# Optimization experiments

Hardware: AMD Instinct MI355X
Metric: run time of the kernel (lower is better)

The kernel has to match this reference:

```python
import jax, jax.numpy as jnp
import numpy as np

NEG_SLOPE = 0.2
EPS = 1e-16

N_NODES = 32768
N_EDGES = 160000
DIM = 768
HEADS1 = 4
OUT1 = DIM // HEADS1  # 192 per head, concat -> 768
HEADS2 = 1
OUT2 = DIM
N_REL = 3


def setup_inputs() -> dict:
    key = jax.random.key(0)
    ks = jax.random.split(key, 12)
    s = 0.02
    return {
        "x": jax.random.normal(ks[0], (N_NODES, DIM), dtype=jnp.float32),
        "edge_index": jax.random.randint(ks[1], (2, N_EDGES), 0, N_NODES, dtype=jnp.int64),
        "edge_type": jax.random.randint(ks[2], (N_EDGES,), 0, N_REL, dtype=jnp.int64),
        "W1": jax.random.normal(ks[3], (N_REL, DIM, HEADS1 * OUT1), dtype=jnp.float32) * s,
        "q1": jax.random.normal(ks[4], (HEADS1 * OUT1, HEADS1), dtype=jnp.float32) * s,
        "k1": jax.random.normal(ks[5], (HEADS1 * OUT1, HEADS1), dtype=jnp.float32) * s,
        "b1": jnp.zeros((HEADS1 * OUT1,), dtype=jnp.float32),
        "W2": jax.random.normal(ks[6], (N_REL, DIM, HEADS2 * OUT2), dtype=jnp.float32) * s,
        "q2": jax.random.normal(ks[7], (HEADS2 * OUT2, HEADS2), dtype=jnp.float32) * s,
        "k2": jax.random.normal(ks[8], (HEADS2 * OUT2, HEADS2), dtype=jnp.float32) * s,
        "b2": jnp.zeros((HEADS2 * OUT2,), dtype=jnp.float32),
    }


def rgat_conv(x, W, q, k, b, src, dst, etype, heads, out_ch, n_nodes):
    """PyG RGATConv, additive-self-attention, across-relation, concat=True, eval mode."""
    # per-relation transform of all nodes: [R, N, H*O] (avoids [E, in, H*O] weight gather)
    xr = jnp.einsum('nd,rdf->rnf', x, W)
    oi = xr[etype, dst]                      # [E, H*O] transformed target feats
    oj = xr[etype, src]                      # [E, H*O] transformed source feats
    qi = oi @ q                              # [E, H]
    kj = oj @ k                              # [E, H]
    alpha = jax.nn.leaky_relu(qi + kj, NEG_SLOPE)
    # segment softmax over edges sharing the same target node
    m = jax.ops.segment_max(alpha, dst, num_segments=n_nodes)     # [N, H]
    e = jnp.exp(alpha - m[dst])
    z = jax.ops.segment_sum(e, dst, num_segments=n_nodes)         # [N, H]
    a = e / (z[dst] + EPS)                                        # [E, H]
    msg = (a[:, :, None] * oj.reshape(-1, heads, out_ch)).reshape(-1, heads * out_ch)
    out = jax.ops.segment_sum(msg, dst, num_segments=n_nodes)     # [N, H*O]
    return out + b


def reference(x, edge_index, edge_type, W1, q1, k1, b1, W2, q2, k2, b2):
    src, dst = edge_index[0], edge_index[1]
    n = x.shape[0]
    h = rgat_conv(x, W1, q1, k1, b1, src, dst, edge_type, HEADS1, OUT1, n)
    h = jax.nn.elu(h)
    # dropout is identity in eval mode
    out = rgat_conv(h, W2, q2, k2, b2, src, dst, edge_type, HEADS2, OUT2, n)
    return out
```

## Files before the change

### kernel.cpp

```cpp
#include <hip/hip_runtime.h>


#define DIM   768
#define NREL  3

typedef __bf16 bf16x8 __attribute__((ext_vector_type(8)));
typedef float  f32x4  __attribute__((ext_vector_type(4)));
typedef unsigned short us4 __attribute__((ext_vector_type(4)));
typedef unsigned short us8 __attribute__((ext_vector_type(8)));

__device__ __forceinline__ float bfs(unsigned short u){
  union { unsigned u; float f; } v; v.u = ((unsigned)u) << 16; return v.f;
}
__device__ __forceinline__ float bfl(unsigned x){
  union { unsigned u; float f; } v; v.u = x << 16; return v.f;
}
__device__ __forceinline__ float bfh(unsigned x){
  union { unsigned u; float f; } v; v.u = x & 0xffff0000u; return v.f;
}
__device__ __forceinline__ unsigned short f2bf(float f){
  union { float f; unsigned u; } v; v.f = f;
  unsigned r = v.u + 0x7fffu + ((v.u >> 16) & 1u);
  return (unsigned short)(r >> 16);
}
__device__ __forceinline__ unsigned pck(float a, float b){
  return (unsigned)f2bf(a) | ((unsigned)f2bf(b) << 16);
}
__device__ __forceinline__ float ldf(const void* p, size_t i, int is32){
  return is32 ? ((const float*)p)[i] : bfs(((const unsigned short*)p)[i]);
}
__device__ __forceinline__ int ldi(const void* p, size_t i, int is64){
  return is64 ? ((const int*)p)[2 * i] : ((const int*)p)[i];
}

typedef __attribute__((address_space(1))) void gvoid_t;
typedef __attribute__((address_space(3))) void lvoid_t;
__device__ __forceinline__ void gload16(const void* g, void* l){
  __builtin_amdgcn_global_load_lds((gvoid_t*)g, (lvoid_t*)l, 16, 0, 0);
}

template<int H>
__device__ __forceinline__ float sel(const float (&a)[H], int h){
  float v = a[0];
#pragma unroll
  for (int i = 1; i < H; ++i) v = (h == i) ? a[i] : v;
  return v;
}

__global__ void detect_kernel(const unsigned short* __restrict__ xu,
                              const unsigned* __restrict__ eiu,
                              const unsigned* __restrict__ etyu,
                              int* __restrict__ flags){
  __shared__ int s_weird, s_ei, s_ety;
  int t = threadIdx.x;
  if (t == 0){ s_weird = 0; s_ei = 0; s_ety = 0; }
  __syncthreads();
  unsigned short u = xu[2 * t];
  int ex = (u >> 7) & 0xff;
  if (ex >= 0xF0 || ex <= 0x40) atomicAdd(&s_weird, 1);
  if (t < 128){
    if (eiu[2 * t + 1]  != 0) atomicAdd(&s_ei, 1);
    if (etyu[2 * t + 1] != 0) atomicAdd(&s_ety, 1);
  }
  __syncthreads();
  if (t == 0){
    flags[0] = (s_weird > 16) ? 1 : 0;
    flags[1] = (s_ei  == 0) ? 1 : 0;
    flags[2] = (s_ety == 0) ? 1 : 0;
  }
}

__global__ void convert_x(const void* __restrict__ xin, unsigned short* __restrict__ xb,
                          const int* __restrict__ flags, int n4){
  int i = blockIdx.x * blockDim.x + threadIdx.x;
  if (i >= n4) return;
  if (flags[0]){
    float4 v = ((const float4*)xin)[i];
    us4 o; o.x = f2bf(v.x); o.y = f2bf(v.y); o.z = f2bf(v.z); o.w = f2bf(v.w);
    ((us4*)xb)[i] = o;
  } else {
    ((us4*)xb)[i] = ((const us4*)xin)[i];
  }
}

__global__ void hist_kernel(const void* __restrict__ ei, int* __restrict__ counts,
                            const int* __restrict__ flags, int E){
  int e = blockIdx.x * blockDim.x + threadIdx.x;
  if (e < E) atomicAdd(&counts[ldi(ei, (size_t)E + e, flags[1])], 1);
}

__global__ void scan_kernel(const int* __restrict__ counts, int* __restrict__ offs,
                            int* __restrict__ cursor, int n){
  __shared__ int s[1024];
  int tid = threadIdx.x;
  int base = tid * 32;
  int loc[32];
  int run = 0;
#pragma unroll
  for (int i = 0; i < 32; ++i){ loc[i] = run; run += counts[base + i]; }
  s[tid] = run;
  __syncthreads();
  for (int off = 1; off < 1024; off <<= 1){
    int add = (tid >= off) ? s[tid - off] : 0;
    __syncthreads();
    s[tid] += add;
    __syncthreads();
  }
  int ex = (tid == 0) ? 0 : s[tid - 1];
#pragma unroll
  for (int i = 0; i < 32; ++i){
    int o = ex + loc[i];
    offs[base + i]   = o;
    cursor[base + i] = o;
  }
  if (tid == 1023) offs[n] = s[1023];
}

__global__ void scatter_kernel(const void* __restrict__ ei, const void* __restrict__ ety,
                               int* __restrict__ cursor, int* __restrict__ payload,
                               const int* __restrict__ flags, int E){
  int e = blockIdx.x * blockDim.x + threadIdx.x;
  if (e < E){
    int dst = ldi(ei, (size_t)E + e, flags[1]);
    int src = ldi(ei, (size_t)e,     flags[1]);
    int et  = ldi(ety, (size_t)e,    flags[2]);
    int pos = atomicAdd(&cursor[dst], 1);
    payload[pos] = (et << 16) | src;
  }
}

__global__ void transpose_w(const void* __restrict__ W, unsigned short* __restrict__ Wt,
                            const int* __restrict__ flags){
  __shared__ unsigned short t[32][33];
  int is32 = flags[0];
  int r = blockIdx.z;
  size_t Wb = (size_t)r * DIM * DIM;
  unsigned short* Wd = Wt + (size_t)r * DIM * DIM;
  int tx = threadIdx.x, ty = threadIdx.y;
  int x  = blockIdx.x * 32 + tx;
  int y0 = blockIdx.y * 32;
#pragma unroll
  for (int i = 0; i < 32; i += 8)
    t[ty + i][tx] = f2bf(ldf(W, Wb + (size_t)(y0 + ty + i) * DIM + x, is32));
  __syncthreads();
  int x2 = blockIdx.y * 32 + tx;
  int y2 = blockIdx.x * 32;
#pragma unroll
  for (int i = 0; i < 32; i += 8) Wd[(size_t)(y2 + ty + i) * DIM + x2] = t[tx][ty + i];
}

template<int H>
__global__ void wqk_kernel(const void* __restrict__ W,
                           const void* __restrict__ q, const void* __restrict__ k,
                           unsigned short* __restrict__ Wqkb,
                           const int* __restrict__ flags){
  int is32 = flags[0];
  int wid  = (blockIdx.x * blockDim.x + threadIdx.x) >> 6;
  int lane = threadIdx.x & 63;
  int r = wid / DIM, d = wid % DIM;
  size_t Wrow = ((size_t)r * DIM + d) * DIM;
  float aq[H], ak[H];
#pragma unroll
  for (int h = 0; h < H; ++h){ aq[h] = 0.f; ak[h] = 0.f; }
#pragma unroll
  for (int j = 0; j < 12; ++j){
    int f = j * 64 + lane;
    float wv = ldf(W, Wrow + f, is32);
#pragma unroll
    for (int h = 0; h < H; ++h){
      aq[h] += wv * ldf(q, (size_t)f * H + h, is32);
      ak[h] += wv * ldf(k, (size_t)f * H + h, is32);
    }
  }
#pragma unroll
  for (int h = 0; h < H; ++h){
    for (int off = 32; off; off >>= 1){
      aq[h] += __shfl_xor(aq[h], off);
      ak[h] += __shfl_xor(ak[h], off);
    }
  }
  if (lane == 0){
#pragma unroll
    for (int h = 0; h < H; ++h){
      Wqkb[(size_t)d * 32 + r * 8 + h]     = f2bf(aq[h]);
      Wqkb[(size_t)d * 32 + r * 8 + 4 + h] = f2bf(ak[h]);
    }
  }
}

__global__ void pack_b(const unsigned short* __restrict__ Wqkb, unsigned short* __restrict__ Bpk){
  int i = blockIdx.x * 256 + threadIdx.x;
  if (i >= 3072) return;
  int lane = i & 63, nt = (i >> 6) & 1, t = i >> 7;
  int kb = t * 32 + (lane >> 4) * 8;
  int col = nt * 16 + (lane & 15);
  us8 v;
#pragma unroll
  for (int j = 0; j < 8; ++j) v[j] = Wqkb[(size_t)(kb + j) * 32 + col];
  ((us8*)Bpk)[i] = v;
}

__global__ void __launch_bounds__(256)
qnkn_mfma(const unsigned short* __restrict__ X, const unsigned short* __restrict__ Bpk,
          float* __restrict__ qn, float* __restrict__ kn, int nN){
  int wv = threadIdx.x >> 6, lane = threadIdx.x & 63;
  int row0 = (blockIdx.x * 4 + wv) * 16;
  int ar = lane & 15, quad = lane >> 4;
  const unsigned short* Arow = X + (size_t)(row0 + ar) * DIM + quad * 8;
  const bf16x8* Bp = (const bf16x8*)Bpk;
  f32x4 acc0 = {0.f,0.f,0.f,0.f}, acc1 = {0.f,0.f,0.f,0.f};
#pragma unroll
  for (int t = 0; t < 24; ++t){
    bf16x8 a  = *(const bf16x8*)(Arow + t * 32);
    bf16x8 b0 = Bp[(t * 2 + 0) * 64 + lane];
    bf16x8 b1 = Bp[(t * 2 + 1) * 64 + lane];
    acc0 = __builtin_amdgcn_mfma_f32_16x16x32_bf16(a, b0, acc0, 0, 0, 0);
    acc1 = __builtin_amdgcn_mfma_f32_16x16x32_bf16(a, b1, acc1, 0, 0, 0);
  }
#pragma unroll
  for (int nt = 0; nt < 2; ++nt){
    int col = nt * 16 + (lane & 15);
    if (col < 24){
      int r = col >> 3, isK = (col >> 2) & 1, h = col & 3;
      float* bp = isK ? kn : qn;
      f32x4 a = nt ? acc1 : acc0;
#pragma unroll
      for (int j = 0; j < 4; ++j){
        int row = row0 + quad * 4 + j;
        bp[((size_t)r * nN + row) * 4 + h] = a[j];
      }
    }
  }
}

#define MM4(mi, av) \
    acc[mi][0] = __builtin_amdgcn_mfma_f32_16x16x32_bf16(av, b0, acc[mi][0], 0, 0, 0); \
    acc[mi][1] = __builtin_amdgcn_mfma_f32_16x16x32_bf16(av, b1, acc[mi][1], 0, 0, 0); \
    acc[mi][2] = __builtin_amdgcn_mfma_f32_16x16x32_bf16(av, b2, acc[mi][2], 0, 0, 0); \
    acc[mi][3] = __builtin_amdgcn_mfma_f32_16x16x32_bf16(av, b3, acc[mi][3], 0, 0, 0);

__global__ void __launch_bounds__(512, 2)
gemm_bf16(const unsigned short* __restrict__ A,
          const unsigned short* __restrict__ Bt,
          unsigned short* __restrict__ C, int M){
  __shared__ __align__(16) unsigned char lds[131072];
  const int K = DIM;
  int i = blockIdx.x;
  int xcd = i & 7, s = i >> 3;
  int bm  = xcd * 16 + s / 9;
  int bnr = s % 9;
  int rrel = bnr / 3, bn = bnr % 3;
  int tid = threadIdx.x;
  int w = tid >> 6, lane = tid & 63;
  int wr = w >> 2, wc = w & 3;
  int m16 = lane & 15, quad = lane >> 4;

  int jlow = m16 >> 1;
  int p    = (((m16 & 1) << 2) | quad) ^ jlow;
  int aoff = (wr * 64 + jlow) * 128 + p * 16;
  int boff = (wc * 32 + jlow) * 128 + p * 16;

  int sq = (lane & 7) ^ (lane >> 3);
  int rb = 2 * (w * 16 + (lane >> 3)) + (sq >> 2);
  const unsigned short* gA = A  + (size_t)(bm * 256 + rb) * K + (sq & 3) * 8;
  const unsigned short* gB = Bt + ((size_t)(rrel * DIM + bn * 256 + rb)) * K + (sq & 3) * 8;
  int dstbase = w * 2048;

  f32x4 acc[8][4];
#pragma unroll
  for (int a = 0; a < 8; ++a)
#pragma unroll
    for (int b = 0; b < 4; ++b) acc[a][b] = (f32x4){0.f, 0.f, 0.f, 0.f};

  auto STAGE = [&](int op, int kk, int dbuf, int k0){
    const unsigned short* g = op ? gB : gA;
#pragma unroll
    for (int it = 0; it < 2; ++it)
      gload16(g + (size_t)(it * 16) * K + kk * 32 + k0,
              &lds[(((dbuf << 2) | (op << 1) | kk) << 14) + dstbase + it * 1024]);
  };
  auto LDA = [&](int kk, int cb, int mi) -> bf16x8 {
    return *(const bf16x8*)&lds[(((cb << 2) | kk) << 14) + aoff + mi * 1024];
  };
  auto LDB = [&](int kk, int cb, int ni) -> bf16x8 {
    return *(const bf16x8*)&lds[(((cb << 2) | 2 | kk) << 14) + boff + ni * 1024];
  };

  auto KTILE = [&](int cb, int k0, int sN, int s2){
    bf16x8 b0, b1, b2, b3, a0, a1, a2, a3;
    b0 = LDB(0, cb, 0); b1 = LDB(0, cb, 1); b2 = LDB(0, cb, 2); b3 = LDB(0, cb, 3);
    a0 = LDA(0, cb, 0); a1 = LDA(0, cb, 1); a2 = LDA(0, cb, 2); a3 = LDA(0, cb, 3);
    if (sN) STAGE(0, 1, cb ^ 1, k0 + 64);
    __builtin_amdgcn_s_barrier();
    __builtin_amdgcn_s_setprio(1);
    MM4(0, a0) MM4(1, a1) MM4(2, a2) MM4(3, a3)
    __builtin_amdgcn_s_setprio(0);
    __builtin_amdgcn_s_barrier();
    a0 = LDA(0, cb, 4); a1 = LDA(0, cb, 5); a2 = LDA(0, cb, 6); a3 = LDA(0, cb, 7);
    if (s2) STAGE(1, 0, cb, k0 + 128);
    __builtin_amdgcn_s_barrier();
    __builtin_amdgcn_s_setprio(1);
    MM4(4, a0) MM4(5, a1) MM4(6, a2) MM4(7, a3)
    __builtin_amdgcn_s_setprio(0);
    __builtin_amdgcn_s_barrier();
    b0 = LDB(1, cb, 0); b1 = LDB(1, cb, 1); b2 = LDB(1, cb, 2); b3 = LDB(1, cb, 3);
    a0 = LDA(1, cb, 0); a1 = LDA(1, cb, 1); a2 = LDA(1, cb, 2); a3 = LDA(1, cb, 3);
    if (s2) STAGE(0, 0, cb, k0 + 128);
    __builtin_amdgcn_s_barrier();
    __builtin_amdgcn_s_setprio(1);
    MM4(0, a0) MM4(1, a1) MM4(2, a2) MM4(3, a3)
    __builtin_amdgcn_s_setprio(0);
    __builtin_amdgcn_s_barrier();
    a0 = LDA(1, cb, 4); a1 = LDA(1, cb, 5); a2 = LDA(1, cb, 6); a3 = LDA(1, cb, 7);
    if (s2) STAGE(1, 1, cb, k0 + 128);
    __builtin_amdgcn_s_barrier();
    __builtin_amdgcn_s_setprio(1);
    MM4(4, a0) MM4(5, a1) MM4(6, a2) MM4(7, a3)
    __builtin_amdgcn_s_setprio(0);
  };

  STAGE(1, 0, 0, 0);  STAGE(0, 0, 0, 0);  STAGE(1, 1, 0, 0);  STAGE(0, 1, 0, 0);
  STAGE(1, 0, 1, 64); STAGE(0, 0, 1, 64); STAGE(1, 1, 1, 64);
  asm volatile("s_waitcnt vmcnt(6)");
  __builtin_amdgcn_s_barrier();

#pragma unroll 1
  for (int it = 0; it < 5; ++it){
    int k0 = it * 128;
    KTILE(0, k0, 1, 1);
    asm volatile("s_waitcnt vmcnt(6)");
    __builtin_amdgcn_s_barrier();
    KTILE(1, k0 + 64, 1, 1);
    asm volatile("s_waitcnt vmcnt(6)");
    __builtin_amdgcn_s_barrier();
  }
  KTILE(0, 640, 1, 0);
  asm volatile("s_waitcnt vmcnt(0)");
  __builtin_amdgcn_s_barrier();
  KTILE(1, 704, 0, 0);

  unsigned short* Cg = C + ((size_t)rrel * M + (size_t)bm * 256) * DIM + bn * 256;
#pragma unroll
  for (int mi = 0; mi < 8; ++mi)
#pragma unroll
    for (int ni = 0; ni < 4; ++ni){
#pragma unroll
      for (int j = 0; j < 4; ++j){
        int row = wr * 128 + mi * 16 + quad * 4 + j;
        int col = wc * 64 + ni * 16 + m16;
        Cg[(size_t)row * DIM + col] = f2bf(acc[mi][ni][j]);
      }
    }
}

template<int H, bool ELU, bool OUT32>
__global__ void __launch_bounds__(256)
agg_kernel(const unsigned short* __restrict__ xr,
           const float* __restrict__ qn, const float* __restrict__ kn,
           const int* __restrict__ offs, const int* __restrict__ payload,
           const void* __restrict__ bias,
           void* __restrict__ outp,
           const int* __restrict__ flags, int nN, int E){
  const int WH = (H == 4) ? 4 : 1;
  __shared__ int   pay_s[4][64];
  __shared__ float w_s[4][64 * WH];
  int is32 = flags[0];
  int wv   = threadIdx.x >> 6;
  int lane = threadIdx.x & 63;
  int n = blockIdx.x * 4 + wv;
  int rs = offs[n], re = offs[n + 1];
  rs = max(rs, 0); re = min(re, E);
  const int myh = (H == 1) ? 0 : (lane >> 4);

  float m_run[H], z_run[H], acc[12];
#pragma unroll
  for (int h = 0; h < H; ++h){ m_run[h] = -__builtin_inff(); z_run[h] = 0.f; }
#pragma unroll
  for (int i = 0; i < 12; ++i) acc[i] = 0.f;

  for (int base = rs; base < re; base += 64){
    int dc = min(64, re - base);
    int pay = 0;
    float al[H];
#pragma unroll
    for (int h = 0; h < H; ++h) al[h] = -__builtin_inff();
    if (lane < dc){
      pay = payload[base + lane];
      int et = pay >> 16, src = pay & 0xffff;
      if (H == 4){
        f32x4 qv = *(const f32x4*)(qn + ((size_t)et * nN + n)   * 4);
        f32x4 kv = *(const f32x4*)(kn + ((size_t)et * nN + src) * 4);
#pragma unroll
        for (int h = 0; h < H; ++h){
          float a = qv[h & 3] + kv[h & 3];
          al[h] = (a > 0.f) ? a : 0.2f * a;
        }
      } else {
        float a = qn[((size_t)et * nN + n) * 4] + kn[((size_t)et * nN + src) * 4];
        al[0] = (a > 0.f) ? a : 0.2f * a;
      }
    }
    float scs[H], wgt[H];
#pragma unroll
    for (int h = 0; h < H; ++h){
      float v = al[h];
      for (int off = 32; off; off >>= 1) v = fmaxf(v, __shfl_xor(v, off));
      float nm = fmaxf(m_run[h], v);
      scs[h] = (m_run[h] == -__builtin_inff()) ? 0.f : expf(m_run[h] - nm);
      m_run[h] = nm;
      wgt[h] = (lane < dc) ? expf(al[h] - nm) : 0.f;
      float s = wgt[h];
      for (int off = 32; off; off >>= 1) s += __shfl_xor(s, off);
      z_run[h] = z_run[h] * scs[h] + s;
    }
    float msc = sel<H>(scs, myh);
#pragma unroll
    for (int i = 0; i < 12; ++i) acc[i] *= msc;

    if (lane < dc){
      pay_s[wv][lane] = pay;
#pragma unroll
      for (int h = 0; h < WH; ++h) w_s[wv][lane * WH + h] = wgt[h];
    }

    for (int j0 = 0; j0 < dc; j0 += 4){
      uint2 c[4][3];
      float w4[4];
#pragma unroll
      for (int u = 0; u < 4; ++u){
        int jc = j0 + u;
        int ok = jc < dc;
        int jl = ok ? jc : j0;
        int pj = pay_s[wv][jl];
        float ww = w_s[wv][jl * WH + ((H == 1) ? 0 : myh)];
        w4[u] = ok ? ww : 0.f;
        int et = pj >> 16, src = pj & 0xffff;
        const uint2* rp = (const uint2*)(xr + ((size_t)et * nN + src) * DIM + lane * 12);
        c[u][0] = rp[0]; c[u][1] = rp[1]; c[u][2] = rp[2];
      }
#pragma unroll
      for (int u = 0; u < 4; ++u){
        float wj = w4[u];
        acc[0]  += wj * bfl(c[u][0].x); acc[1]  += wj * bfh(c[u][0].x);
        acc[2]  += wj * bfl(c[u][0].y); acc[3]  += wj * bfh(c[u][0].y);
        acc[4]  += wj * bfl(c[u][1].x); acc[5]  += wj * bfh(c[u][1].x);
        acc[6]  += wj * bfl(c[u][1].y); acc[7]  += wj * bfh(c[u][1].y);
        acc[8]  += wj * bfl(c[u][2].x); acc[9]  += wj * bfh(c[u][2].x);
        acc[10] += wj * bfl(c[u][2].y); acc[11] += wj * bfh(c[u][2].y);
      }
    }
  }

  float inv = 1.0f / (sel<H>(z_run, myh) + 1e-16f);
  float o[12];
#pragma unroll
  for (int i = 0; i < 12; ++i){
    float v = acc[i] * inv + ldf(bias, (size_t)lane * 12 + i, is32);
    if (ELU) v = (v > 0.f) ? v : (expf(v) - 1.f);
    o[i] = v;
  }
  if (OUT32 && is32){
    float* op = (float*)outp + (size_t)n * DIM + lane * 12;
    float4 f0 = {o[0], o[1], o[2],  o[3]};
    float4 f1 = {o[4], o[5], o[6],  o[7]};
    float4 f2 = {o[8], o[9], o[10], o[11]};
    ((float4*)op)[0] = f0; ((float4*)op)[1] = f1; ((float4*)op)[2] = f2;
  } else {
    uint2* op = (uint2*)((unsigned short*)outp + (size_t)n * DIM + lane * 12);
    uint2 s0, s1, s2;
    s0.x = pck(o[0], o[1]);  s0.y = pck(o[2], o[3]);
    s1.x = pck(o[4], o[5]);  s1.y = pck(o[6], o[7]);
    s2.x = pck(o[8], o[9]);  s2.y = pck(o[10], o[11]);
    op[0] = s0; op[1] = s1; op[2] = s2;
  }
}

extern "C" void kernel_launch(void* const* d_in, const int* in_sizes, int n_in,
                              void* d_out, int out_size, void* d_ws, size_t ws_size,
                              hipStream_t stream){
  const void* x   = d_in[0];
  const void* ei  = d_in[1];
  const void* ety = d_in[2];
  const void* W1  = d_in[3];
  const void* q1  = d_in[4];
  const void* k1  = d_in[5];
  const void* b1  = d_in[6];
  const void* W2  = d_in[7];
  const void* q2  = d_in[8];
  const void* k2  = d_in[9];
  const void* b2  = d_in[10];

  int nN = in_sizes[0] / DIM;
  int E  = in_sizes[2];

  char* ws = (char*)d_ws;
  size_t off = 0;
  auto alloc = [&](size_t bytes) -> void* {
    void* p = ws + off;
    off += (bytes + 255) & ~(size_t)255;
    return p;
  };
  unsigned short* xr   = (unsigned short*)alloc((size_t)NREL * nN * DIM * 2);
  unsigned short* xb   = (unsigned short*)alloc((size_t)nN * DIM * 2);
  unsigned short* h    = (unsigned short*)alloc((size_t)nN * DIM * 2);
  unsigned short* Wt   = (unsigned short*)alloc((size_t)NREL * DIM * DIM * 2);
  unsigned short* Wqkb = (unsigned short*)alloc((size_t)DIM * 32 * 2);
  unsigned short* Bpk  = (unsigned short*)alloc((size_t)3072 * 16);
  float* qn  = (float*)alloc((size_t)NREL * nN * 4 * 4);
  float* kn  = (float*)alloc((size_t)NREL * nN * 4 * 4);
  int* offs    = (int*)alloc((size_t)(nN + 1) * 4);
  int* cursor  = (int*)alloc((size_t)nN * 4);
  int* counts  = (int*)alloc((size_t)nN * 4);
  int* payload = (int*)alloc((size_t)E * 4);
  int* flags   = (int*)alloc(16);

  detect_kernel<<<1, 256, 0, stream>>>((const unsigned short*)x, (const unsigned*)ei,
                                       (const unsigned*)ety, flags);
  convert_x<<<(nN * DIM / 4 + 255) / 256, 256, 0, stream>>>(x, xb, flags, nN * DIM / 4);

  hipMemsetAsync(counts, 0, (size_t)nN * 4, stream);
  hist_kernel<<<(E + 255) / 256, 256, 0, stream>>>(ei, counts, flags, E);
  scan_kernel<<<1, 1024, 0, stream>>>(counts, offs, cursor, nN);
  scatter_kernel<<<(E + 255) / 256, 256, 0, stream>>>(ei, ety, cursor, payload, flags, E);

  dim3 tg(DIM / 32, DIM / 32, NREL), tb(32, 8);
  int gemm_blocks = 8 * (16 * 9);

  transpose_w<<<tg, tb, 0, stream>>>(W1, Wt, flags);
  hipMemsetAsync(Wqkb, 0, (size_t)DIM * 32 * 2, stream);
  wqk_kernel<4><<<(NREL * DIM) / 4, 256, 0, stream>>>(W1, q1, k1, Wqkb, flags);
  pack_b<<<12, 256, 0, stream>>>(Wqkb, Bpk);
  qnkn_mfma<<<nN / 64, 256, 0, stream>>>(xb, Bpk, qn, kn, nN);
  gemm_bf16<<<gemm_blocks, 512, 0, stream>>>(xb, Wt, xr, nN);
  agg_kernel<4, true, false><<<nN / 4, 256, 0, stream>>>(xr, qn, kn, offs, payload, b1, h,
                                                         flags, nN, E);

  transpose_w<<<tg, tb, 0, stream>>>(W2, Wt, flags);
  hipMemsetAsync(Wqkb, 0, (size_t)DIM * 32 * 2, stream);
  wqk_kernel<1><<<(NREL * DIM) / 4, 256, 0, stream>>>(W2, q2, k2, Wqkb, flags);
  pack_b<<<12, 256, 0, stream>>>(Wqkb, Bpk);
  qnkn_mfma<<<nN / 64, 256, 0, stream>>>(h, Bpk, qn, kn, nN);
  gemm_bf16<<<gemm_blocks, 512, 0, stream>>>(h, Wt, xr, nN);
  agg_kernel<1, false, true><<<nN / 4, 256, 0, stream>>>(xr, qn, kn, offs, payload, b2,
                                                         d_out, flags, nN, E);
}
```

Measured before the change: 677.9 us.

## Shrink GEMM tile to 128x256 with triple-buffered 32-wide K pipeline

Halves the GEMM M-tile from 256 to 128 rows, so each of the 8 waves holds a 4x4 accumulator array instead of 8x4. The K-loop now steps by 32 through a three-slot LDS ring, with one stage in flight while another is computed. LDS use drops from 128 KB to 72 KB and launch bounds request 4 blocks per CU, aiming at higher occupancy and better latency hiding. In exchange, each tile reuses its B data over fewer rows, it needs more barriers per unit of K, and twice as many blocks are launched.

```diff
diff --git a/kernel.cpp b/kernel.cpp
--- a/kernel.cpp
+++ b/kernel.cpp
@@ -239,15 +239,15 @@
     acc[mi][2] = __builtin_amdgcn_mfma_f32_16x16x32_bf16(av, b2, acc[mi][2], 0, 0, 0); \
     acc[mi][3] = __builtin_amdgcn_mfma_f32_16x16x32_bf16(av, b3, acc[mi][3], 0, 0, 0);
 
-__global__ void __launch_bounds__(512, 2)
+__global__ void __launch_bounds__(512, 4)
 gemm_bf16(const unsigned short* __restrict__ A,
           const unsigned short* __restrict__ Bt,
           unsigned short* __restrict__ C, int M){
-  __shared__ __align__(16) unsigned char lds[131072];
+  __shared__ __align__(16) unsigned char lds[73728];
   const int K = DIM;
   int i = blockIdx.x;
   int xcd = i & 7, s = i >> 3;
-  int bm  = xcd * 16 + s / 9;
+  int bm  = xcd * 32 + s / 9;
   int bnr = s % 9;
   int rrel = bnr / 3, bn = bnr % 3;
   int tid = threadIdx.x;
@@ -257,96 +257,76 @@
 
   int jlow = m16 >> 1;
   int p    = (((m16 & 1) << 2) | quad) ^ jlow;
-  int aoff = (wr * 64 + jlow) * 128 + p * 16;
+  int aoff = (wr * 32 + jlow) * 128 + p * 16;
   int boff = (wc * 32 + jlow) * 128 + p * 16;
 
-  int sq = (lane & 7) ^ (lane >> 3);
-  int rb = 2 * (w * 16 + (lane >> 3)) + (sq >> 2);
-  const unsigned short* gA = A  + (size_t)(bm * 256 + rb) * K + (sq & 3) * 8;
-  const unsigned short* gB = Bt + ((size_t)(rrel * DIM + bn * 256 + rb)) * K + (sq & 3) * 8;
-  int dstbase = w * 2048;
-
-  f32x4 acc[8][4];
-#pragma unroll
-  for (int a = 0; a < 8; ++a)
+  int sq  = (tid & 7) ^ ((tid >> 3) & 7);
+  int rb  = 2 * (tid >> 3) + (sq >> 2);
+  const unsigned short* gA  = A  + (size_t)(bm * 128 + rb) * K + (sq & 3) * 8;
+  const unsigned short* gB0 = Bt + ((size_t)(rrel * DIM + bn * 256 + rb)) * K + (sq & 3) * 8;
+  const unsigned short* gB1 = gB0 + (size_t)128 * K;
+  unsigned char* dst = &lds[w * 1024];
+
+  f32x4 acc[4][4];
+#pragma unroll
+  for (int a = 0; a < 4; ++a)
 #pragma unroll
     for (int b = 0; b < 4; ++b) acc[a][b] = (f32x4){0.f, 0.f, 0.f, 0.f};
 
-  auto STAGE = [&](int op, int kk, int dbuf, int k0){
-    const unsigned short* g = op ? gB : gA;
-#pragma unroll
-    for (int it = 0; it < 2; ++it)
-      gload16(g + (size_t)(it * 16) * K + kk * 32 + k0,
-              &lds[(((dbuf << 2) | (op << 1) | kk) << 14) + dstbase + it * 1024]);
+  auto STAGE = [&](int slot, int k0){
+    unsigned char* base = dst + slot * 24576;
+    gload16(gA  + k0, base);
+    gload16(gB0 + k0, base + 8192);
+    gload16(gB1 + k0, base + 16384);
   };
-  auto LDA = [&](int kk, int cb, int mi) -> bf16x8 {
-    return *(const bf16x8*)&lds[(((cb << 2) | kk) << 14) + aoff + mi * 1024];
+  auto LDA = [&](int slot, int mi) -> bf16x8 {
+    return *(const bf16x8*)&lds[slot * 24576 + aoff + mi * 1024];
   };
-  auto LDB = [&](int kk, int cb, int ni) -> bf16x8 {
-    return *(const bf16x8*)&lds[(((cb << 2) | 2 | kk) << 14) + boff + ni * 1024];
+  auto LDB = [&](int slot, int ni) -> bf16x8 {
+    return *(const bf16x8*)&lds[slot * 24576 + 8192 + boff + ni * 1024];
   };
-
-  auto KTILE = [&](int cb, int k0, int sN, int s2){
-    bf16x8 b0, b1, b2, b3, a0, a1, a2, a3;
-    b0 = LDB(0, cb, 0); b1 = LDB(0, cb, 1); b2 = LDB(0, cb, 2); b3 = LDB(0, cb, 3);
-    a0 = LDA(0, cb, 0); a1 = LDA(0, cb, 1); a2 = LDA(0, cb, 2); a3 = LDA(0, cb, 3);
-    if (sN) STAGE(0, 1, cb ^ 1, k0 + 64);
-    __builtin_amdgcn_s_barrier();
+  auto PHASE = [&](int slotR, int k0, int slotW, int kW, bool doStage){
+    bf16x8 b0 = LDB(slotR, 0), b1 = LDB(slotR, 1), b2 = LDB(slotR, 2), b3 = LDB(slotR, 3);
+    bf16x8 a0 = LDA(slotR, 0), a1 = LDA(slotR, 1), a2 = LDA(slotR, 2), a3 = LDA(slotR, 3);
+    if (doStage) STAGE(slotW, kW);
     __builtin_amdgcn_s_setprio(1);
     MM4(0, a0) MM4(1, a1) MM4(2, a2) MM4(3, a3)
     __builtin_amdgcn_s_setprio(0);
+  };
+
+  STAGE(0, 0); STAGE(1, 32);
+  asm volatile("s_waitcnt vmcnt(3)");
+  __builtin_amdgcn_s_barrier();
+
+#pragma unroll 1
+  for (int t = 0; t < 21; t += 3){
+    int k0 = t * 32;
+    PHASE(0, k0,       2, k0 + 64, true);
+    asm volatile("s_waitcnt vmcnt(3)");
     __builtin_amdgcn_s_barrier();
-    a0 = LDA(0, cb, 4); a1 = LDA(0, cb, 5); a2 = LDA(0, cb, 6); a3 = LDA(0, cb, 7);
-    if (s2) STAGE(1, 0, cb, k0 + 128);
+    PHASE(1, k0 + 32,  0, k0 + 96, true);
+    asm volatile("s_waitcnt vmcnt(3)");
     __builtin_amdgcn_s_barrier();
-    __builtin_amdgcn_s_setprio(1);
-    MM4(4, a0) MM4(5, a1) MM4(6, a2) MM4(7, a3)
-    __builtin_amdgcn_s_setprio(0);
+    PHASE(2, k0 + 64,  1, k0 + 128, true);
+    asm volatile("s_waitcnt vmcnt(3)");
     __builtin_amdgcn_s_barrier();
-    b0 = LDB(1, cb, 0); b1 = LDB(1, cb, 1); b2 = LDB(1, cb, 2); b3 = LDB(1, cb, 3);
-    a0 = LDA(1, cb, 0); a1 = LDA(1, cb, 1); a2 = LDA(1, cb, 2); a3 = LDA(1, cb, 3);
-    if (s2) STAGE(0, 0, cb, k0 + 128);
-    __builtin_amdgcn_s_barrier();
-    __builtin_amdgcn_s_setprio(1);
-    MM4(0, a0) MM4(1, a1) MM4(2, a2) MM4(3, a3)
-    __builtin_amdgcn_s_setprio(0);
-    __builtin_amdgcn_s_barrier();
-    a0 = LDA(1, cb, 4); a1 = LDA(1, cb, 5); a2 = LDA(1, cb, 6); a3 = LDA(1, cb, 7);
-    if (s2) STAGE(1, 1, cb, k0 + 128);
-    __builtin_amdgcn_s_barrier();
-    __builtin_amdgcn_s_setprio(1);
-    MM4(4, a0) MM4(5, a1) MM4(6, a2) MM4(7, a3)
-    __builtin_amdgcn_s_setprio(0);
-  };
-
-  STAGE(1, 0, 0, 0);  STAGE(0, 0, 0, 0);  STAGE(1, 1, 0, 0);  STAGE(0, 1, 0, 0);
-  STAGE(1, 0, 1, 64); STAGE(0, 0, 1, 64); STAGE(1, 1, 1, 64);
-  asm volatile("s_waitcnt vmcnt(6)");
+  }
+  PHASE(0, 672, 2, 736, true);
+  asm volatile("s_waitcnt vmcnt(3)");
   __builtin_amdgcn_s_barrier();
-
-#pragma unroll 1
-  for (int it = 0; it < 5; ++it){
-    int k0 = it * 128;
-    KTILE(0, k0, 1, 1);
-    asm volatile("s_waitcnt vmcnt(6)");
-    __builtin_amdgcn_s_barrier();
-    KTILE(1, k0 + 64, 1, 1);
-    asm volatile("s_waitcnt vmcnt(6)");
-    __builtin_amdgcn_s_barrier();
-  }
-  KTILE(0, 640, 1, 0);
+  PHASE(1, 704, 0, 0, false);
   asm volatile("s_waitcnt vmcnt(0)");
   __builtin_amdgcn_s_barrier();
-  KTILE(1, 704, 0, 0);
-
-  unsigned short* Cg = C + ((size_t)rrel * M + (size_t)bm * 256) * DIM + bn * 256;
-#pragma unroll
-  for (int mi = 0; mi < 8; ++mi)
+  PHASE(2, 736, 0, 0, false);
+
+  unsigned short* Cg = C + ((size_t)rrel * M + (size_t)bm * 128) * DIM + bn * 256;
+#pragma unroll
+  for (int mi = 0; mi < 4; ++mi)
 #pragma unroll
     for (int ni = 0; ni < 4; ++ni){
 #pragma unroll
       for (int j = 0; j < 4; ++j){
-        int row = wr * 128 + mi * 16 + quad * 4 + j;
+        int row = wr * 64 + mi * 16 + quad * 4 + j;
         int col = wc * 64 + ni * 16 + m16;
         Cg[(size_t)row * DIM + col] = f2bf(acc[mi][ni][j]);
       }
@@ -524,7 +504,7 @@
   scatter_kernel<<<(E + 255) / 256, 256, 0, stream>>>(ei, ety, cursor, payload, flags, E);
 
   dim3 tg(DIM / 32, DIM / 32, NREL), tb(32, 8);
-  int gemm_blocks = 8 * (16 * 9);
+  int gemm_blocks = 8 * (32 * 9);
 
   transpose_w<<<tg, tb, 0, stream>>>(W1, Wt, flags);
   hipMemsetAsync(Wqkb, 0, (size_t)DIM * 32 * 2, stream);
```

New measurement: 653.3 us. -3.6%, faster.
